# Kernel tuning notes

Hardware: AMD Instinct MI355X
Metric: run time of the kernel (lower is better)

The kernel has to match this reference:

```python
import jax, jax.numpy as jnp
import numpy as np

KH = KW = 3
DH = DW = 1

def _extract_patches(x, kh, kw, dh, dw):
    # x: [B, C, H, W] -> patches: [B, C, OH, OW, kh*kw] matching torch unfold order
    B, C, H, W = x.shape
    oh = (H - kh) // dh + 1
    ow = (W - kw) // dw + 1
    cols = []
    for i in range(kh):
        for j in range(kw):
            cols.append(x[:, :, i:i + oh * dh:dh, j:j + ow * dw:dw])
    return jnp.stack(cols, axis=-1)  # [B, C, OH, OW, k*k]


def setup_inputs() -> dict:
    key = jax.random.key(0)
    k1, k2 = jax.random.split(key)
    x = jax.random.normal(k1, (64, 32, 64, 64), dtype=jnp.float32)
    weight = jax.random.normal(k2, (1, 64, 32, 62, 62, 9), dtype=jnp.float32)
    return {"x": x, "weight": weight}


def reference(x, weight):
    # patches: [B, Cin, OH, OW, K2]; weight[0]: [Cout, Cin, OH, OW, K2]
    patches = _extract_patches(x, KH, KW, DH, DW)
    # per-location dot product over (Cin, K2) -> [B, Cout, OH, OW]
    out = jnp.einsum('bihwk,oihwk->bohw', patches, weight[0])
    return out
```

## Files before the change

kernel.cpp:

```cpp
#include <hip/hip_runtime.h>


#define OW 62
#define LOCS 3844
#define WSTRIDE_I 34596u
#define XM 131072u

__global__ void lc2d_transpose_x(const float* __restrict__ x, float* __restrict__ xT) {
    __shared__ float tile[64][65];
    const int m0 = blockIdx.x * 64;
    const int t = threadIdx.x;
    const int c = t & 63, q = t >> 6;
#pragma unroll
    for (int j = 0; j < 16; ++j) {
        const int b = q * 16 + j;
        tile[c][b] = x[(size_t)b * XM + (size_t)(m0 + c)];
    }
    __syncthreads();
#pragma unroll
    for (int j = 0; j < 16; ++j) {
        const int m = q * 16 + j;
        xT[(size_t)(m0 + m) * 64u + (size_t)c] = tile[m][c];
    }
}

__global__ __launch_bounds__(512) void lc2d_main(const float* __restrict__ w,
                                                 const float* __restrict__ xT,
                                                 float* __restrict__ out) {
    __shared__ float Wl[2][8][8][128];

    const int bid = blockIdx.x;
    const int oh  = bid >> 3;
    const int t8  = bid & 7;
    const int ow0 = (t8 < 7) ? (t8 << 3) : 54;
    const int loc0 = oh * OW + ow0;

    const int lane = threadIdx.x & 63;
    const int g = __builtin_amdgcn_readfirstlane((int)(threadIdx.x >> 6));
    const int lclamp = (lane > 7) ? 7 : lane;

    auto stage = [&](int ib, int i) {
#pragma unroll
        for (int op = 0; op < 8; ++op) {
            const size_t rb = (size_t)((g * 8 + op) * 32 + i) * WSTRIDE_I + (size_t)loc0 * 9u;
            const float* g1 = w + rb + (size_t)lane;
            const float* g2 = w + rb + 64u + (size_t)lclamp;
            __builtin_amdgcn_global_load_lds(
                (const __attribute__((address_space(1))) unsigned int*)g1,
                (__attribute__((address_space(3))) unsigned int*)&Wl[ib][g][op][0], 4, 0, 0);
            __builtin_amdgcn_global_load_lds(
                (const __attribute__((address_space(1))) unsigned int*)g2,
                (__attribute__((address_space(3))) unsigned int*)&Wl[ib][g][op][64], 4, 0, 0);
        }
    };

    float acc[8][8];
#pragma unroll
    for (int a = 0; a < 8; ++a)
#pragma unroll
        for (int bb = 0; bb < 8; ++bb) acc[a][bb] = 0.f;

    stage(0, 0);

#pragma unroll 1
    for (int i = 0; i < 32; ++i) {
        float xr[30];
        const float* xp = xT + ((size_t)i * 4096u + (size_t)oh * 64u + (size_t)ow0) * 64u + (size_t)lane;
#pragma unroll
        for (int r = 0; r < 3; ++r)
#pragma unroll
            for (int c = 0; c < 10; ++c)
                xr[r * 10 + c] = xp[(size_t)((r * 64 + c) * 64)];

        if (i < 31) stage((i + 1) & 1, i + 1);

        asm volatile("s_waitcnt vmcnt(16)" ::: "memory");
        __builtin_amdgcn_sched_barrier(0);

        const int ib = i & 1;
#pragma unroll
        for (int op = 0; op < 8; ++op) {
            const float* wrow = &Wl[ib][g][op][0];
#pragma unroll
            for (int q = 0; q < 18; ++q) {
                const float4 wq = *(const float4*)(wrow + (q << 2));
#pragma unroll
                for (int u = 0; u < 4; ++u) {
                    const int f = (q << 2) + u;
                    const int l = f / 9;
                    const int k = f - 9 * l;
                    const float wf = (u == 0) ? wq.x : (u == 1) ? wq.y : (u == 2) ? wq.z : wq.w;
                    acc[op][l] = fmaf(wf, xr[(k / 3) * 10 + l + (k % 3)], acc[op][l]);
                }
            }
        }
    }

#pragma unroll
    for (int op = 0; op < 8; ++op) {
        float* po = out + (size_t)(lane * 64 + g * 8 + op) * (size_t)LOCS + (size_t)loc0;
#pragma unroll
        for (int q = 0; q < 4; ++q) {
            float2 v = make_float2(acc[op][q * 2], acc[op][q * 2 + 1]);
            *(float2*)(po + q * 2) = v;
        }
    }
}

extern "C" void kernel_launch(void* const* d_in, const int* in_sizes, int n_in,
                              void* d_out, int out_size, void* d_ws, size_t ws_size,
                              hipStream_t stream) {
    const float* x = (const float*)d_in[0];
    const float* w = (const float*)d_in[1];
    float* out = (float*)d_out;
    float* xT = (float*)d_ws;

    lc2d_transpose_x<<<dim3(XM / 64), dim3(256), 0, stream>>>(x, xT);
    lc2d_main<<<dim3(496), dim3(512), 0, stream>>>(w, xT, out);
}
```

Before: 324.4 us.

## Replace LDS-staged weight loads with uniform scalar register loads and smaller tiles

Drops the LDS double buffer filled by global_load_lds. Each wave now loads its weight rows through wave-uniform (readfirstlane) addresses into registers, so the compiler can use scalar loads, and software-pipelines one output channel ahead. The tile shrinks from 8 to 4 output columns, doubling the grid to 992 blocks with a permuted block-to-tile mapping. The x window is double-buffered across input channels. The kernel is bound by streaming the weights, so the gain depends on whether scalar loads keep up and on overlapping 4-column tiles re-reading x.

```diff
diff --git a/kernel.cpp b/kernel.cpp
--- a/kernel.cpp
+++ b/kernel.cpp
@@ -1,9 +1,8 @@
 #include <hip/hip_runtime.h>
 
 
-#define OW 62
+#define OWDIM 62
 #define LOCS 3844
-#define WSTRIDE_I 34596u
 #define XM 131072u
 
 __global__ void lc2d_transpose_x(const float* __restrict__ x, float* __restrict__ xT) {
@@ -24,86 +23,78 @@
     }
 }
 
-__global__ __launch_bounds__(512) void lc2d_main(const float* __restrict__ w,
-                                                 const float* __restrict__ xT,
-                                                 float* __restrict__ out) {
-    __shared__ float Wl[2][8][8][128];
-
+__global__ __launch_bounds__(512, 4) void lc2d_main(const float* __restrict__ w,
+                                                    const float* __restrict__ xT,
+                                                    float* __restrict__ out) {
     const int bid = blockIdx.x;
-    const int oh  = bid >> 3;
-    const int t8  = bid & 7;
-    const int ow0 = (t8 < 7) ? (t8 << 3) : 54;
-    const int loc0 = oh * OW + ow0;
+    const int tile = (bid & 7) * 124 + (bid >> 3);
+    const int oh = tile >> 4;
+    const int t4 = tile & 15;
+    const int ow0 = (t4 < 15) ? (t4 << 2) : 58;
+    const int loc0 = oh * OWDIM + ow0;
 
     const int lane = threadIdx.x & 63;
     const int g = __builtin_amdgcn_readfirstlane((int)(threadIdx.x >> 6));
-    const int lclamp = (lane > 7) ? 7 : lane;
 
-    auto stage = [&](int ib, int i) {
+    float acc[8][4];
+#pragma unroll
+    for (int a = 0; a < 8; ++a)
+#pragma unroll
+        for (int l = 0; l < 4; ++l) acc[a][l] = 0.f;
+
+    float xrA[18], xrB[18];
+    float wsP[36], wsQ[36];
+
+    auto woff = [&](int i, int op) -> int {
+        const int o = g * 8 + op;
+        return __builtin_amdgcn_readfirstlane(((o * 32 + i) * LOCS + loc0) * 9);
+    };
+    auto load36 = [&](float* ws, int off) {
+        const float* p = w + (size_t)off;
+#pragma unroll
+        for (int j = 0; j < 36; ++j) ws[j] = p[j];
+    };
+    auto loadx = [&](float* xr, int i) {
+        const float* xp = xT + (((size_t)i * 4096u + (size_t)(oh * 64 + ow0)) << 6) + (size_t)lane;
+#pragma unroll
+        for (int r = 0; r < 3; ++r)
+#pragma unroll
+            for (int c = 0; c < 6; ++c)
+                xr[r * 6 + c] = xp[(size_t)((r * 4096 + c * 64))];
+    };
+
+    auto octet = [&](int i, const float* xr) {
 #pragma unroll
         for (int op = 0; op < 8; ++op) {
-            const size_t rb = (size_t)((g * 8 + op) * 32 + i) * WSTRIDE_I + (size_t)loc0 * 9u;
-            const float* g1 = w + rb + (size_t)lane;
-            const float* g2 = w + rb + 64u + (size_t)lclamp;
-            __builtin_amdgcn_global_load_lds(
-                (const __attribute__((address_space(1))) unsigned int*)g1,
-                (__attribute__((address_space(3))) unsigned int*)&Wl[ib][g][op][0], 4, 0, 0);
-            __builtin_amdgcn_global_load_lds(
-                (const __attribute__((address_space(1))) unsigned int*)g2,
-                (__attribute__((address_space(3))) unsigned int*)&Wl[ib][g][op][64], 4, 0, 0);
+            const float* cur = (op & 1) ? wsQ : wsP;
+            float* nxt = (op & 1) ? wsP : wsQ;
+            const int ni = (op == 7) ? i + 1 : i;
+            const int nop = (op + 1) & 7;
+            if (ni < 32) load36(nxt, woff(ni, nop));
+#pragma unroll
+            for (int l = 0; l < 4; ++l)
+#pragma unroll
+                for (int k = 0; k < 9; ++k)
+                    acc[op][l] = fmaf(cur[l * 9 + k], xr[(k / 3) * 6 + l + (k % 3)], acc[op][l]);
         }
     };
 
-    float acc[8][8];
-#pragma unroll
-    for (int a = 0; a < 8; ++a)
-#pragma unroll
-        for (int bb = 0; bb < 8; ++bb) acc[a][bb] = 0.f;
-
-    stage(0, 0);
+    load36(wsP, woff(0, 0));
+    loadx(xrA, 0);
 
 #pragma unroll 1
-    for (int i = 0; i < 32; ++i) {
-        float xr[30];
-        const float* xp = xT + ((size_t)i * 4096u + (size_t)oh * 64u + (size_t)ow0) * 64u + (size_t)lane;
-#pragma unroll
-        for (int r = 0; r < 3; ++r)
-#pragma unroll
-            for (int c = 0; c < 10; ++c)
-                xr[r * 10 + c] = xp[(size_t)((r * 64 + c) * 64)];
-
-        if (i < 31) stage((i + 1) & 1, i + 1);
-
-        asm volatile("s_waitcnt vmcnt(16)" ::: "memory");
-        __builtin_amdgcn_sched_barrier(0);
-
-        const int ib = i & 1;
-#pragma unroll
-        for (int op = 0; op < 8; ++op) {
-            const float* wrow = &Wl[ib][g][op][0];
-#pragma unroll
-            for (int q = 0; q < 18; ++q) {
-                const float4 wq = *(const float4*)(wrow + (q << 2));
-#pragma unroll
-                for (int u = 0; u < 4; ++u) {
-                    const int f = (q << 2) + u;
-                    const int l = f / 9;
-                    const int k = f - 9 * l;
-                    const float wf = (u == 0) ? wq.x : (u == 1) ? wq.y : (u == 2) ? wq.z : wq.w;
-                    acc[op][l] = fmaf(wf, xr[(k / 3) * 10 + l + (k % 3)], acc[op][l]);
-                }
-            }
-        }
+    for (int i = 0; i < 32; i += 2) {
+        loadx(xrB, i + 1);
+        octet(i, xrA);
+        if (i + 2 < 32) loadx(xrA, i + 2);
+        octet(i + 1, xrB);
     }
 
 #pragma unroll
     for (int op = 0; op < 8; ++op) {
         float* po = out + (size_t)(lane * 64 + g * 8 + op) * (size_t)LOCS + (size_t)loc0;
-#pragma unroll
-        for (int q = 0; q < 4; ++q) {
-            float2 v = make_float2(acc[op][q * 2], acc[op][q * 2 + 1]);
-            *(float2*)(po + q * 2) = v;
-        }
+        *(float2*)(po + 0) = make_float2(acc[op][0], acc[op][1]);
+        *(float2*)(po + 2) = make_float2(acc[op][2], acc[op][3]);
     }
 }
 
@@ -116,5 +107,5 @@
     float* xT = (float*)d_ws;
 
     lc2d_transpose_x<<<dim3(XM / 64), dim3(256), 0, stream>>>(x, xT);
-    lc2d_main<<<dim3(496), dim3(512), 0, stream>>>(w, xT, out);
+    lc2d_main<<<dim3(992), dim3(512), 0, stream>>>(w, xT, out);
 }
```

Result: slower. 864.3 us (+166.4%).
